# Optimization experiments

Measured on AMD Instinct MI355X. Metric: run time of the kernel, lower is better.

The kernel has to match this reference:

```python
import jax, jax.numpy as jnp
import numpy as np

Q_DIM = 256; KV_DIM = 256; C = 32; N_HEAD = 8; OUT_DIM = 256
B1, B2, LQ, LK = 1, 128, 256, 256


def _glorot(key, shape, gain=1.0):
    fan_in, fan_out = shape[-2], shape[-1]
    std = gain * np.sqrt(2.0 / float(fan_in + fan_out))
    dev = np.sqrt(3.0) * std
    return jax.random.uniform(key, shape, jnp.float32, -dev, dev)


def setup_inputs() -> dict:
    key = jax.random.key(0)
    ks = jax.random.split(key, 12)
    q_data = jax.random.normal(ks[0], (B1, B2, LQ, Q_DIM), jnp.float32)
    kv_data = jax.random.normal(ks[1], (B1, B2, LK, KV_DIM), jnp.float32)
    bias = jax.random.normal(ks[2], (B1, B2, N_HEAD, LQ, LK), jnp.float32)
    nonbatched_bias = jax.random.normal(ks[3], (B1, N_HEAD, LQ, LK), jnp.float32)
    # torch Linear weights are [out, in]; original init is zeros but we use
    # glorot for a non-degenerate numerical baseline.
    Wq = _glorot(ks[4], (N_HEAD * C, Q_DIM))
    Wk = _glorot(ks[5], (N_HEAD * C, KV_DIM))
    Wv = _glorot(ks[6], (N_HEAD * C, KV_DIM))
    Wg = _glorot(ks[7], (N_HEAD * C, Q_DIM))
    bg = jnp.ones((N_HEAD * C,), jnp.float32)  # bias_init=1.0
    Wo = _glorot(ks[8], (OUT_DIM, N_HEAD * C))
    bo = jnp.zeros((OUT_DIM,), jnp.float32)
    return dict(q_data=q_data, kv_data=kv_data, bias=bias,
                nonbatched_bias=nonbatched_bias, Wq=Wq, Wk=Wk, Wv=Wv,
                Wg=Wg, bg=bg, Wo=Wo, bo=bo)


def reference(q_data, kv_data, bias, nonbatched_bias, Wq, Wk, Wv, Wg, bg, Wo, bo):
    c = C
    # projections: [b1,b2,len,n_head,c]
    q = (q_data @ Wq.T).reshape(*q_data.shape[:-1], N_HEAD, c) * (c ** -0.5)
    k = (kv_data @ Wk.T).reshape(*kv_data.shape[:-1], N_HEAD, c)
    v = (kv_data @ Wv.T).reshape(*kv_data.shape[:-1], N_HEAD, c)
    # logits: [b1,b2,n_head,len_q,len_kv]
    logits = jnp.einsum('bsqhc,bskhc->bshqk', q, k)
    logits = logits + bias + nonbatched_bias[:, None]
    weights = jax.nn.softmax(logits, axis=-1)
    weighted_avg = jnp.einsum('bshqk,bskhc->bsqhc', weights, v)
    gate = jax.nn.sigmoid((q_data @ Wg.T + bg).reshape(*q_data.shape[:-1], N_HEAD, c))
    weighted_avg = weighted_avg * gate
    out = weighted_avg.reshape(*weighted_avg.shape[:-2], N_HEAD * c) @ Wo.T + bo
    return out
```

## Files before the change

### kernel.cpp

```cpp
#include <hip/hip_runtime.h>
#include <hip/hip_bf16.h>

#define NB2 128
#define LQK 256
#define DIM 256
#define NH 8
#define CC 32

typedef __bf16 bf16x8 __attribute__((ext_vector_type(8)));
typedef __bf16 bf16x4 __attribute__((ext_vector_type(4)));
typedef float f32x4 __attribute__((ext_vector_type(4)));

#define MFMA16 __builtin_amdgcn_mfma_f32_16x16x32_bf16

#define TP 72

#define NTOK ((size_t)NB2 * LQK * NH * CC)

static __device__ __forceinline__ void gload_lds16(const void* g, void* l) {
    __builtin_amdgcn_global_load_lds(
        (const __attribute__((address_space(1))) unsigned int*)g,
        (__attribute__((address_space(3))) unsigned int*)l,
        16, 0, 0);
}

__global__ __launch_bounds__(256) void k_cvt(
    const float* __restrict__ qd, const float* __restrict__ kvd,
    const float* __restrict__ Wq, const float* __restrict__ Wk,
    const float* __restrict__ Wv, const float* __restrict__ Wg,
    const float* __restrict__ Wo,
    __bf16* __restrict__ qbf, __bf16* __restrict__ kvbf,
    __bf16* __restrict__ wBF)
{
    const int b = blockIdx.x;
    if (b < 8192) {
        size_t i = ((size_t)b * 256 + threadIdx.x) * 8;
        const float* src;
        __bf16* dst;
        if (i < NTOK) { src = qd + i; dst = qbf + i; }
        else          { src = kvd + (i - NTOK); dst = kvbf + (i - NTOK); }
        f32x4 a = *(const f32x4*)src;
        f32x4 c = *(const f32x4*)(src + 4);
        bf16x8 r;
        r[0] = (__bf16)a[0]; r[1] = (__bf16)a[1]; r[2] = (__bf16)a[2]; r[3] = (__bf16)a[3];
        r[4] = (__bf16)c[0]; r[5] = (__bf16)c[1]; r[6] = (__bf16)c[2]; r[7] = (__bf16)c[3];
        *(bf16x8*)dst = r;
    } else {
        int i = ((b - 8192) * 256 + threadIdx.x) * 4;
        int mat = i >> 16;
        int off = i & 65535;
        const float* src = (mat == 0) ? Wq : (mat == 1) ? Wk : (mat == 2) ? Wv
                          : (mat == 3) ? Wg : Wo;
        f32x4 v = *(const f32x4*)(src + off);
        __bf16* d = wBF + ((size_t)mat << 16) + off;
        d[0] = (__bf16)v[0]; d[1] = (__bf16)v[1]; d[2] = (__bf16)v[2]; d[3] = (__bf16)v[3];
    }
}

__global__ __launch_bounds__(256, 2) void k_proj(
    const __bf16* __restrict__ qbf, const __bf16* __restrict__ kvbf,
    const __bf16* __restrict__ wBF, const float* __restrict__ bg,
    __bf16* __restrict__ wsq, __bf16* __restrict__ wsk,
    __bf16* __restrict__ wsvT, __bf16* __restrict__ wsgT)
{
    __shared__ __bf16 At[2][128 * 64];
    __shared__ __bf16 Bt[2][128 * 64];

    const int mb = blockIdx.x, nb = blockIdx.y;
    const int t = nb >> 1;
    const __bf16* X = (t == 0 || t == 3) ? qbf : kvbf;
    const __bf16* W = wBF + ((size_t)t << 16) + (size_t)((nb & 1) * 128) * 256;

    const int tid = threadIdx.x;
    const int lane = tid & 63, w = tid >> 6;
    const int g = lane >> 4, c0 = lane & 15;
    const int mq = (w >> 1) * 64, nq = (w & 1) * 64;
    const int m0 = mb * 128;
    const int lrow = lane >> 3, lu = lane & 7;

    auto stage = [&](int buf, int kt) {
#pragma unroll
        for (int i = 0; i < 4; i++) {
            const int rr = i * 32 + w * 8 + lrow;
            const int su = lu ^ (rr & 7);
            gload_lds16(X + (size_t)(m0 + rr) * 256 + kt * 64 + su * 8,
                        &At[buf][(i * 4 + w) * 512]);
        }
#pragma unroll
        for (int i = 0; i < 4; i++) {
            const int rr = i * 32 + w * 8 + lrow;
            const int su = lu ^ (rr & 7);
            gload_lds16(W + (size_t)rr * 256 + kt * 64 + su * 8,
                        &Bt[buf][(i * 4 + w) * 512]);
        }
    };

    f32x4 acc[4][4] = {};
    stage(0, 0);
    __syncthreads();

#pragma unroll
    for (int kt = 0; kt < 4; kt++) {
        const int cur = kt & 1;
        if (kt < 3) stage(cur ^ 1, kt + 1);
#pragma unroll
        for (int ks = 0; ks < 2; ks++) {
            const int px = ((ks * 4 + g) ^ (c0 & 7)) * 8;
            bf16x8 af[4], bf_[4];
#pragma unroll
            for (int mi = 0; mi < 4; mi++)
                af[mi] = *(const bf16x8*)(&At[cur][(mq + mi * 16 + c0) * 64 + px]);
#pragma unroll
            for (int ni = 0; ni < 4; ni++)
                bf_[ni] = *(const bf16x8*)(&Bt[cur][(nq + ni * 16 + c0) * 64 + px]);
#pragma unroll
            for (int mi = 0; mi < 4; mi++)
#pragma unroll
                for (int ni = 0; ni < 4; ni++)
                    acc[mi][ni] = MFMA16(af[mi], bf_[ni], acc[mi][ni], 0, 0, 0);
        }
        __syncthreads();
    }

#pragma unroll
    for (int ni = 0; ni < 4; ni++) {
        const int nloc = (nb & 1) * 128 + nq + ni * 16 + c0;
        const int h = nloc >> 5, c = nloc & 31;
        const float bg_ = (t == 3) ? bg[nloc] : 0.0f;
#pragma unroll
        for (int mi = 0; mi < 4; mi++) {
            const int mbase = m0 + mq + mi * 16 + g * 4;
            const int b2 = mbase >> 8;
            if (t == 2) {
                bf16x4 pk;
#pragma unroll
                for (int reg = 0; reg < 4; reg++) pk[reg] = (__bf16)acc[mi][ni][reg];
                *(bf16x4*)(&wsvT[((size_t)(b2 * NH + h) * CC + c) * LQK + (mbase & 255)]) = pk;
            } else if (t == 3) {
                bf16x4 pk;
#pragma unroll
                for (int reg = 0; reg < 4; reg++)
                    pk[reg] = (__bf16)(1.0f / (1.0f + __expf(-(acc[mi][ni][reg] + bg_))));
                *(bf16x4*)(&wsgT[((size_t)(b2 * NH + h) * CC + c) * LQK + (mbase & 255)]) = pk;
            } else {
#pragma unroll
                for (int reg = 0; reg < 4; reg++) {
                    const int l = (mbase + reg) & 255;
                    float v = acc[mi][ni][reg];
                    size_t idx = ((size_t)(b2 * NH + h) * LQK + l) * CC + c;
                    if (t == 0) wsq[idx] = (__bf16)(v * 0.17677669529663689f);
                    else        wsk[idx] = (__bf16)v;
                }
            }
        }
    }
}

__global__ __launch_bounds__(256, 3) void k_attn(
    const __bf16* __restrict__ wsq, const __bf16* __restrict__ wsk,
    const __bf16* __restrict__ wsvT, const __bf16* __restrict__ wsgT,
    const float* __restrict__ bias, const float* __restrict__ nbb,
    __bf16* __restrict__ wswa)
{
    __shared__ float  Bl[2][16][256];
    __shared__ __bf16 P[4][16][TP];
    __shared__ float  lsum[4][16];
    __shared__ float  op[4][16][33];

    const int tid = threadIdx.x;
    const int u0 = blockIdx.x;
    const int xcd = u0 & 7, slot = u0 >> 3;
    const int head = xcd + 8 * (slot >> 2);
    const int qt = slot & 3;
    const int b2 = head >> 3, h = head & 7;

    const int lane = tid & 63, w = tid >> 6;
    const int g = lane >> 4, kg = g * 8, c0 = lane & 15;

    const __bf16* qp = wsq + (size_t)(b2 * NH + h) * LQK * CC;
    const __bf16* kp = wsk + (size_t)(b2 * NH + h) * LQK * CC;
    const __bf16* vT = wsvT + (size_t)(b2 * NH + h) * CC * LQK;
    const __bf16* gT = wsgT + (size_t)(b2 * NH + h) * CC * LQK;
    const float* npb = nbb + (size_t)h * LQK * LQK;
    const float* bblk = bias + ((size_t)(b2 * NH + h) * LQK + qt * 64) * LQK;

    auto stage = [&](int buf, int p) {
#pragma unroll
        for (int i = 0; i < 4; i++) {
            const int row = w * 4 + i;
            gload_lds16(bblk + (size_t)(p * 16 + row) * LQK + ((lane ^ row) * 4),
                        &Bl[buf][row][0]);
        }
    };

    bf16x8 kf[4], vf[4];
#pragma unroll
    for (int j = 0; j < 4; j++)
        kf[j] = *(const bf16x8*)(kp + (size_t)(w * 64 + j * 16 + c0) * CC + kg);
#pragma unroll
    for (int kt2 = 0; kt2 < 2; kt2++)
#pragma unroll
        for (int vn = 0; vn < 2; vn++)
            vf[kt2 * 2 + vn] = *(const bf16x8*)(
                vT + (size_t)(vn * 16 + c0) * LQK + w * 64 + kt2 * 32 + kg);

    const int ridx = tid * 2;
    const int rqr = ridx >> 5;
    const int rcb = ridx & 31;

    bf16x8 qfb[2];
    f32x4 nb4b[2][4];
    float gab[2], gbb[2];
    auto loadregs = [&](int buf, int p) {
        const int qglob = qt * 64 + p * 16 + c0;
        qfb[buf] = *(const bf16x8*)(qp + (size_t)qglob * CC + kg);
#pragma unroll
        for (int j = 0; j < 4; j++)
            nb4b[buf][j] = *(const f32x4*)(npb + (size_t)qglob * LQK + w * 64 + j * 16 + g * 4);
        const int qg = qt * 64 + p * 16 + rqr;
        gab[buf] = (float)gT[(size_t)rcb * LQK + qg];
        gbb[buf] = (float)gT[(size_t)(rcb + 1) * LQK + qg];
    };

    stage(0, 0);
    loadregs(0, 0);
    __syncthreads();

#pragma unroll
    for (int p = 0; p < 4; p++) {
        const int cur = p & 1;

        if (p < 3) {
            stage(cur ^ 1, p + 1);
            loadregs(cur ^ 1, p + 1);
        }
        __builtin_amdgcn_sched_barrier(0);

        float csum = 0.0f;
#pragma unroll
        for (int j = 0; j < 4; j++) {
            f32x4 b4 = *(const f32x4*)(&Bl[cur][c0][(w * 16 + ((j * 4 + g) ^ c0)) * 4]);
            f32x4 cc;
#pragma unroll
            for (int r2 = 0; r2 < 4; r2++) cc[r2] = b4[r2] + nb4b[cur][j][r2];
            f32x4 s = MFMA16(kf[j], qfb[cur], cc, 0, 0, 0);
            bf16x4 pk;
#pragma unroll
            for (int r2 = 0; r2 < 4; r2++) {
                float e = __expf(s[r2]);
                csum += e;
                pk[r2] = (__bf16)e;
            }
            *(bf16x4*)(&P[w][c0][j * 16 + g * 4]) = pk;
        }
        csum += __shfl_xor(csum, 16);
        csum += __shfl_xor(csum, 32);
        if (lane < 16) lsum[w][lane] = csum;

        f32x4 o2[2] = {};
#pragma unroll
        for (int kt2 = 0; kt2 < 2; kt2++) {
            bf16x8 pa = *(const bf16x8*)(&P[w][c0][kt2 * 32 + kg]);
#pragma unroll
            for (int vn = 0; vn < 2; vn++)
                o2[vn] = MFMA16(pa, vf[kt2 * 2 + vn], o2[vn], 0, 0, 0);
        }
#pragma unroll
        for (int vn = 0; vn < 2; vn++)
#pragma unroll
            for (int r2 = 0; r2 < 4; r2++)
                op[w][g * 4 + r2][vn * 16 + c0] = o2[vn][r2];

        __syncthreads();

        {
            const int qg = qt * 64 + p * 16 + rqr;
            const float li = 1.0f / (lsum[0][rqr] + lsum[1][rqr] + lsum[2][rqr] + lsum[3][rqr]);
            float v0 = op[0][rqr][rcb] + op[1][rqr][rcb] + op[2][rqr][rcb] + op[3][rqr][rcb];
            float v1 = op[0][rqr][rcb + 1] + op[1][rqr][rcb + 1] + op[2][rqr][rcb + 1] + op[3][rqr][rcb + 1];
            v0 *= li * gab[cur];
            v1 *= li * gbb[cur];
            __bf16* dst = &wswa[((size_t)(b2 * LQK + qg)) * (NH * CC) + h * CC + rcb];
            dst[0] = (__bf16)v0;
            dst[1] = (__bf16)v1;
        }
        __syncthreads();
    }
}

__global__ __launch_bounds__(256, 2) void k_out(
    const __bf16* __restrict__ wa, const __bf16* __restrict__ wBF,
    const float* __restrict__ bo, float* __restrict__ out)
{
    __shared__ __bf16 At[2][128 * 64];
    __shared__ __bf16 Bt[2][128 * 64];

    const int mb = blockIdx.x, nb = blockIdx.y;
    const __bf16* W = wBF + ((size_t)4 << 16) + (size_t)(nb * 128) * 256;

    const int tid = threadIdx.x;
    const int lane = tid & 63, w = tid >> 6;
    const int g = lane >> 4, c0 = lane & 15;
    const int mq = (w >> 1) * 64, nq = (w & 1) * 64;
    const int m0 = mb * 128;
    const int lrow = lane >> 3, lu = lane & 7;

    auto stage = [&](int buf, int kt) {
#pragma unroll
        for (int i = 0; i < 4; i++) {
            const int rr = i * 32 + w * 8 + lrow;
            const int su = lu ^ (rr & 7);
            gload_lds16(wa + (size_t)(m0 + rr) * 256 + kt * 64 + su * 8,
                        &At[buf][(i * 4 + w) * 512]);
        }
#pragma unroll
        for (int i = 0; i < 4; i++) {
            const int rr = i * 32 + w * 8 + lrow;
            const int su = lu ^ (rr & 7);
            gload_lds16(W + (size_t)rr * 256 + kt * 64 + su * 8,
                        &Bt[buf][(i * 4 + w) * 512]);
        }
    };

    f32x4 acc[4][4] = {};
    stage(0, 0);
    __syncthreads();

#pragma unroll
    for (int kt = 0; kt < 4; kt++) {
        const int cur = kt & 1;
        if (kt < 3) stage(cur ^ 1, kt + 1);
#pragma unroll
        for (int ks = 0; ks < 2; ks++) {
            const int px = ((ks * 4 + g) ^ (c0 & 7)) * 8;
            bf16x8 af[4], bf_[4];
#pragma unroll
            for (int mi = 0; mi < 4; mi++)
                af[mi] = *(const bf16x8*)(&At[cur][(mq + mi * 16 + c0) * 64 + px]);
#pragma unroll
            for (int ni = 0; ni < 4; ni++)
                bf_[ni] = *(const bf16x8*)(&Bt[cur][(nq + ni * 16 + c0) * 64 + px]);
#pragma unroll
            for (int mi = 0; mi < 4; mi++)
#pragma unroll
                for (int ni = 0; ni < 4; ni++)
                    acc[mi][ni] = MFMA16(af[mi], bf_[ni], acc[mi][ni], 0, 0, 0);
        }
        __syncthreads();
    }

#pragma unroll
    for (int ni = 0; ni < 4; ni++) {
        const int n = nb * 128 + nq + ni * 16 + c0;
        const float bo_ = bo[n];
#pragma unroll
        for (int mi = 0; mi < 4; mi++) {
            const int mbase = m0 + mq + mi * 16 + g * 4;
#pragma unroll
            for (int reg = 0; reg < 4; reg++)
                out[(size_t)(mbase + reg) * 256 + n] = acc[mi][ni][reg] + bo_;
        }
    }
}

extern "C" void kernel_launch(void* const* d_in, const int* in_sizes, int n_in,
                              void* d_out, int out_size, void* d_ws, size_t ws_size,
                              hipStream_t stream) {
    const float* qd  = (const float*)d_in[0];
    const float* kvd = (const float*)d_in[1];
    const float* bias = (const float*)d_in[2];
    const float* nbb = (const float*)d_in[3];
    const float* Wq = (const float*)d_in[4];
    const float* Wk = (const float*)d_in[5];
    const float* Wv = (const float*)d_in[6];
    const float* Wg = (const float*)d_in[7];
    const float* bg = (const float*)d_in[8];
    const float* Wo = (const float*)d_in[9];
    const float* bo = (const float*)d_in[10];
    float* out = (float*)d_out;

    __bf16* ws = (__bf16*)d_ws;
    __bf16* wsq  = ws;
    __bf16* wsk  = wsq + NTOK;
    __bf16* wsvT = wsk + NTOK;
    __bf16* wsgT = wsvT + NTOK;
    __bf16* wBF  = wsgT + NTOK;
    __bf16* qbf  = wBF + 5 * 65536;
    __bf16* kvbf = qbf + NTOK;
    __bf16* wswa = qbf;

    k_cvt<<<dim3(8512), 256, 0, stream>>>(qd, kvd, Wq, Wk, Wv, Wg, Wo,
                                          qbf, kvbf, wBF);
    k_proj<<<dim3(256, 8), 256, 0, stream>>>(qbf, kvbf, wBF, bg,
                                             wsq, wsk, wsvT, wsgT);
    k_attn<<<dim3(4096), 256, 0, stream>>>(wsq, wsk, wsvT, wsgT, bias, nbb, wswa);
    k_out<<<dim3(256, 2), 256, 0, stream>>>(wswa, wBF, bo, out);
}
```

Measured before the change: 158.9 us.

## Double-buffer attention partial sums to drop a barrier; store gate row-major

```diff
diff --git a/kernel.cpp b/kernel.cpp
--- a/kernel.cpp
+++ b/kernel.cpp
@@ -9,6 +9,7 @@
 
 typedef __bf16 bf16x8 __attribute__((ext_vector_type(8)));
 typedef __bf16 bf16x4 __attribute__((ext_vector_type(4)));
+typedef __bf16 bf16x2 __attribute__((ext_vector_type(2)));
 typedef float f32x4 __attribute__((ext_vector_type(4)));
 
 #define MFMA16 __builtin_amdgcn_mfma_f32_16x16x32_bf16
@@ -61,7 +62,7 @@
     const __bf16* __restrict__ qbf, const __bf16* __restrict__ kvbf,
     const __bf16* __restrict__ wBF, const float* __restrict__ bg,
     __bf16* __restrict__ wsq, __bf16* __restrict__ wsk,
-    __bf16* __restrict__ wsvT, __bf16* __restrict__ wsgT)
+    __bf16* __restrict__ wsvT, __bf16* __restrict__ wsg)
 {
     __shared__ __bf16 At[2][128 * 64];
     __shared__ __bf16 Bt[2][128 * 64];
@@ -136,20 +137,15 @@
 #pragma unroll
                 for (int reg = 0; reg < 4; reg++) pk[reg] = (__bf16)acc[mi][ni][reg];
                 *(bf16x4*)(&wsvT[((size_t)(b2 * NH + h) * CC + c) * LQK + (mbase & 255)]) = pk;
-            } else if (t == 3) {
-                bf16x4 pk;
-#pragma unroll
-                for (int reg = 0; reg < 4; reg++)
-                    pk[reg] = (__bf16)(1.0f / (1.0f + __expf(-(acc[mi][ni][reg] + bg_))));
-                *(bf16x4*)(&wsgT[((size_t)(b2 * NH + h) * CC + c) * LQK + (mbase & 255)]) = pk;
             } else {
 #pragma unroll
                 for (int reg = 0; reg < 4; reg++) {
                     const int l = (mbase + reg) & 255;
                     float v = acc[mi][ni][reg];
                     size_t idx = ((size_t)(b2 * NH + h) * LQK + l) * CC + c;
-                    if (t == 0) wsq[idx] = (__bf16)(v * 0.17677669529663689f);
-                    else        wsk[idx] = (__bf16)v;
+                    if (t == 0)      wsq[idx] = (__bf16)(v * 0.17677669529663689f);
+                    else if (t == 1) wsk[idx] = (__bf16)v;
+                    else             wsg[idx] = (__bf16)(1.0f / (1.0f + __expf(-(v + bg_))));
                 }
             }
         }
@@ -158,14 +154,14 @@
 
 __global__ __launch_bounds__(256, 3) void k_attn(
     const __bf16* __restrict__ wsq, const __bf16* __restrict__ wsk,
-    const __bf16* __restrict__ wsvT, const __bf16* __restrict__ wsgT,
+    const __bf16* __restrict__ wsvT, const __bf16* __restrict__ wsg,
     const float* __restrict__ bias, const float* __restrict__ nbb,
     __bf16* __restrict__ wswa)
 {
     __shared__ float  Bl[2][16][256];
     __shared__ __bf16 P[4][16][TP];
-    __shared__ float  lsum[4][16];
-    __shared__ float  op[4][16][33];
+    __shared__ float  lsum[2][4][16];
+    __shared__ __bf16 op[2][4][16][40];
 
     const int tid = threadIdx.x;
     const int u0 = blockIdx.x;
@@ -180,7 +176,7 @@
     const __bf16* qp = wsq + (size_t)(b2 * NH + h) * LQK * CC;
     const __bf16* kp = wsk + (size_t)(b2 * NH + h) * LQK * CC;
     const __bf16* vT = wsvT + (size_t)(b2 * NH + h) * CC * LQK;
-    const __bf16* gT = wsgT + (size_t)(b2 * NH + h) * CC * LQK;
+    const __bf16* gR = wsg + (size_t)(b2 * NH + h) * LQK * CC;
     const float* npb = nbb + (size_t)h * LQK * LQK;
     const float* bblk = bias + ((size_t)(b2 * NH + h) * LQK + qt * 64) * LQK;
 
@@ -210,7 +206,7 @@
 
     bf16x8 qfb[2];
     f32x4 nb4b[2][4];
-    float gab[2], gbb[2];
+    bf16x2 g2b[2];
     auto loadregs = [&](int buf, int p) {
         const int qglob = qt * 64 + p * 16 + c0;
         qfb[buf] = *(const bf16x8*)(qp + (size_t)qglob * CC + kg);
@@ -218,24 +214,10 @@
         for (int j = 0; j < 4; j++)
             nb4b[buf][j] = *(const f32x4*)(npb + (size_t)qglob * LQK + w * 64 + j * 16 + g * 4);
         const int qg = qt * 64 + p * 16 + rqr;
-        gab[buf] = (float)gT[(size_t)rcb * LQK + qg];
-        gbb[buf] = (float)gT[(size_t)(rcb + 1) * LQK + qg];
-    };
-
-    stage(0, 0);
-    loadregs(0, 0);
-    __syncthreads();
-
-#pragma unroll
-    for (int p = 0; p < 4; p++) {
-        const int cur = p & 1;
-
-        if (p < 3) {
-            stage(cur ^ 1, p + 1);
-            loadregs(cur ^ 1, p + 1);
-        }
-        __builtin_amdgcn_sched_barrier(0);
-
+        g2b[buf] = *(const bf16x2*)(&gR[(size_t)qg * CC + rcb]);
+    };
+
+    auto compute = [&](int cur) {
         float csum = 0.0f;
 #pragma unroll
         for (int j = 0; j < 4; j++) {
@@ -255,7 +237,7 @@
         }
         csum += __shfl_xor(csum, 16);
         csum += __shfl_xor(csum, 32);
-        if (lane < 16) lsum[w][lane] = csum;
+        if (lane < 16) lsum[cur][w][lane] = csum;
 
         f32x4 o2[2] = {};
 #pragma unroll
@@ -269,23 +251,46 @@
         for (int vn = 0; vn < 2; vn++)
 #pragma unroll
             for (int r2 = 0; r2 < 4; r2++)
-                op[w][g * 4 + r2][vn * 16 + c0] = o2[vn][r2];
-
-        __syncthreads();
-
-        {
-            const int qg = qt * 64 + p * 16 + rqr;
-            const float li = 1.0f / (lsum[0][rqr] + lsum[1][rqr] + lsum[2][rqr] + lsum[3][rqr]);
-            float v0 = op[0][rqr][rcb] + op[1][rqr][rcb] + op[2][rqr][rcb] + op[3][rqr][rcb];
-            float v1 = op[0][rqr][rcb + 1] + op[1][rqr][rcb + 1] + op[2][rqr][rcb + 1] + op[3][rqr][rcb + 1];
-            v0 *= li * gab[cur];
-            v1 *= li * gbb[cur];
-            __bf16* dst = &wswa[((size_t)(b2 * LQK + qg)) * (NH * CC) + h * CC + rcb];
-            dst[0] = (__bf16)v0;
-            dst[1] = (__bf16)v1;
-        }
-        __syncthreads();
-    }
+                op[cur][w][g * 4 + r2][vn * 16 + c0] = (__bf16)o2[vn][r2];
+    };
+
+    auto reduce_store = [&](int p, int pb) {
+        const int qg = qt * 64 + p * 16 + rqr;
+        const float li = 1.0f /
+            (lsum[pb][0][rqr] + lsum[pb][1][rqr] + lsum[pb][2][rqr] + lsum[pb][3][rqr]);
+        float v0 = (float)op[pb][0][rqr][rcb]     + (float)op[pb][1][rqr][rcb]
+                 + (float)op[pb][2][rqr][rcb]     + (float)op[pb][3][rqr][rcb];
+        float v1 = (float)op[pb][0][rqr][rcb + 1] + (float)op[pb][1][rqr][rcb + 1]
+                 + (float)op[pb][2][rqr][rcb + 1] + (float)op[pb][3][rqr][rcb + 1];
+        v0 *= li * (float)g2b[pb][0];
+        v1 *= li * (float)g2b[pb][1];
+        __bf16* dst = &wswa[((size_t)(b2 * LQK + qg)) * (NH * CC) + h * CC + rcb];
+        dst[0] = (__bf16)v0;
+        dst[1] = (__bf16)v1;
+    };
+
+    stage(0, 0);
+    loadregs(0, 0);
+    __syncthreads();
+
+    stage(1, 1); loadregs(1, 1);
+    __builtin_amdgcn_sched_barrier(0);
+    compute(0);
+    __syncthreads();
+    reduce_store(0, 0);
+    stage(0, 2); loadregs(0, 2);
+    __builtin_amdgcn_sched_barrier(0);
+    compute(1);
+    __syncthreads();
+    reduce_store(1, 1);
+    stage(1, 3); loadregs(1, 3);
+    __builtin_amdgcn_sched_barrier(0);
+    compute(0);
+    __syncthreads();
+    reduce_store(2, 0);
+    compute(1);
+    __syncthreads();
+    reduce_store(3, 1);
 }
 
 __global__ __launch_bounds__(256, 2) void k_out(
@@ -383,8 +388,8 @@
     __bf16* wsq  = ws;
     __bf16* wsk  = wsq + NTOK;
     __bf16* wsvT = wsk + NTOK;
-    __bf16* wsgT = wsvT + NTOK;
-    __bf16* wBF  = wsgT + NTOK;
+    __bf16* wsg  = wsvT + NTOK;
+    __bf16* wBF  = wsg + NTOK;
     __bf16* qbf  = wBF + 5 * 65536;
     __bf16* kvbf = qbf + NTOK;
     __bf16* wswa = qbf;
@@ -392,7 +397,7 @@
     k_cvt<<<dim3(8512), 256, 0, stream>>>(qd, kvd, Wq, Wk, Wv, Wg, Wo,
                                           qbf, kvbf, wBF);
     k_proj<<<dim3(256, 8), 256, 0, stream>>>(qbf, kvbf, wBF, bg,
-                                             wsq, wsk, wsvT, wsgT);
-    k_attn<<<dim3(4096), 256, 0, stream>>>(wsq, wsk, wsvT, wsgT, bias, nbb, wswa);
+                                             wsq, wsk, wsvT, wsg);
+    k_attn<<<dim3(4096), 256, 0, stream>>>(wsq, wsk, wsvT, wsg, bias, nbb, wswa);
     k_out<<<dim3(256, 2), 256, 0, stream>>>(wswa, wBF, bo, out);
 }
```

Measured after the change: 155.8 us (median of 2 runs). 2.0% less time.
